# Kernel tuning notes

Hardware: AMD Instinct MI355X
Metric: run time of the kernel (lower is better)

Reference implementation:

```python
import jax, jax.numpy as jnp
import numpy as np

NEG = -1e9
TAU = 1.0
N_SAMPLES = 5
SWEEP = (0.1, 0.5, 5)


def layer_norm(x, g, b, eps=1e-5):
    m = x.mean(-1, keepdims=True)
    v = x.var(-1, keepdims=True)
    return (x - m) / jnp.sqrt(v + eps) * g + b


def entmax15(z):
    # exact 1.5-entmax along last axis (Peters & Martins 2019 sort-based algorithm)
    z = z / 2.0
    zs = jnp.sort(z, axis=-1)[..., ::-1]               # descending
    T = z.shape[-1]
    kk = jnp.arange(1, T + 1, dtype=z.dtype)
    mean = jnp.cumsum(zs, -1) / kk
    mean_sq = jnp.cumsum(zs * zs, -1) / kk
    ss = kk * (mean_sq - mean * mean)
    delta = jnp.clip((1.0 - ss) / kk, 0.0)
    tau = mean - jnp.sqrt(delta)
    support = jnp.sum((tau <= zs).astype(jnp.int32), -1, keepdims=True)  # k_star
    tau_star = jnp.take_along_axis(tau, support - 1, axis=-1)
    return jnp.square(jnp.clip(z - tau_star, 0.0))


def stochastic_topk(key, scores, attn, k, tau, n_samples):
    # vectorized over samples AND batch rows with per-row variable k:
    # threshold = k-th largest perturbed score per row (ties measure-zero w/ gumbel)
    u = jax.random.uniform(key, (n_samples,) + scores.shape)
    noise = -jnp.log(-jnp.log(u + 1e-6) + 1e-6)
    pert = jnp.where(attn[None] == 0, NEG, scores[None] + noise * tau)  # [S,B,T]
    srt = jnp.sort(pert, -1)[..., ::-1]
    idx = jnp.broadcast_to((k - 1)[None, :, None], pert.shape[:2] + (1,))
    thr = jnp.take_along_axis(srt, idx, axis=-1)       # [S,B,1]
    h = (pert >= thr).astype(scores.dtype)
    return h.mean(0)                                   # [B,T]


def pool(tok, attn):
    # masked mean pooling (stand-in for sent_encoder.pool)
    return (tok * attn[..., None]).sum(1) / jnp.clip(attn.sum(1, keepdims=True), 1e-6)


def _forward(ids, embeddings, attn, ln_g, ln_b, W1, b1, W2, b2, emb_table):
    emb = embeddings * attn[..., None]
    h = jax.nn.gelu(layer_norm(emb, ln_g, ln_b) @ W1 + b1, approximate=False)
    scores = (h @ W2 + b2)[..., 0]                     # [B,T]
    scores = jnp.where(attn == 0, NEG, scores)

    tok = emb_table[ids]                               # stand-in token embeddings
    full_rep = jax.lax.stop_gradient(pool(tok, attn))  # torch.no_grad path

    T_eff = attn.sum(1)                                # [B]
    # g_soft is identical across the rho sweep in the original; hoisted here
    g_soft = entmax15(scores / TAU) * attn
    g_soft = g_soft / jnp.clip(g_soft.sum(1, keepdims=True), 1e-6)

    key = jax.random.key(42)
    rhos = np.linspace(*SWEEP)
    g_sweep, loss_sweep, rho_eff_sweep = [], [], []
    recon_sum = jnp.zeros((), embeddings.dtype)
    g = None
    for j, rho in enumerate(rhos):
        k = jnp.maximum((float(rho) * T_eff).astype(jnp.int32), 1)
        g_hard = stochastic_topk(jax.random.fold_in(key, j), scores, attn, k, TAU, N_SAMPLES)
        # straight-through: hard forward, soft (entmax) backward
        g = jax.lax.stop_gradient(g_hard) - jax.lax.stop_gradient(g_soft) + g_soft
        rho_eff_sweep.append(g.sum(1) / T_eff)
        eff_attn = attn * g
        pred_rep = pool(tok, eff_attn)
        l_r = jnp.mean(jnp.square(pred_rep - full_rep))  # recon_loss = MSE stand-in
        recon_sum = recon_sum + l_r
        g_sweep.append(g)
        loss_sweep.append(l_r)
    recon_avg = recon_sum / len(rhos)
    return g, jnp.stack(g_sweep), recon_avg, jnp.stack(loss_sweep), jnp.stack(rho_eff_sweep)


def setup_inputs() -> dict:
    key = jax.random.key(0)
    B, T, D, H, V = 8, 2048, 1024, 1365, 32000
    ks = jax.random.split(key, 8)
    return {
        "ids": jax.random.randint(ks[0], (B, T), 0, V),
        "embeddings": jax.random.normal(ks[1], (B, T, D), jnp.float32),
        "attn": jnp.ones((B, T), jnp.float32),
        "ln_g": jnp.ones((D,), jnp.float32),
        "ln_b": jnp.zeros((D,), jnp.float32),
        "W1": jax.random.normal(ks[2], (D, H), jnp.float32) * 0.02,
        "b1": jnp.zeros((H,), jnp.float32),
        "W2": jax.random.normal(ks[3], (H, 1), jnp.float32) * 0.02,
        "b2": jnp.zeros((1,), jnp.float32),
        "emb_table": jax.random.normal(ks[4], (V, D), jnp.float32) * 0.02,
    }


def reference(ids, embeddings, attn, ln_g, ln_b, W1, b1, W2, b2, emb_table):
    return _forward(ids, embeddings, attn, ln_g, ln_b, W1, b1, W2, b2, emb_table)
```

## Files before the change

kernel.cpp:

```cpp
#include <hip/hip_runtime.h>
#include <math.h>
#include <stdint.h>

#define B_ 8
#define T_ 2048
#define D_ 1024
#define H_ 1365
#define HPAD 1536
#define NTOK (B_*T_)
#define NSAMP 5
#define NRHO 5

typedef float  f32x4  __attribute__((ext_vector_type(4)));
typedef __bf16 bf16x8 __attribute__((ext_vector_type(8)));

#define WS_SCORES 0
#define WS_CNT    (WS_SCORES + NTOK*8)
#define WS_PREDW  (WS_CNT + NRHO*B_*T_*4)
#define WS_FULLW  (WS_PREDW + NRHO*B_*D_*8)
#define WS_SUMEFF (WS_FULLW + B_*D_*8)
#define WS_SUMATT (WS_SUMEFF + NRHO*B_*8)
#define WS_SUMG   (WS_SUMATT + B_*8)
#define WS_ZERO_BYTES (WS_SUMG + NRHO*B_*8)
#define WS_STATS  (WS_SUMG + NRHO*B_*8)
#define WS_W1THI  (WS_STATS + NTOK*8)
#define WS_W1TLO  (WS_W1THI + (size_t)HPAD*D_*2)
#define WS_AHI    (WS_W1TLO + (size_t)HPAD*D_*2)
#define WS_ALO    (WS_AHI + (size_t)NTOK*D_*2)
#define WS_FULL_END (WS_ALO + (size_t)NTOK*D_*2)

#define OUT_G      0
#define OUT_GSW    16384
#define OUT_RECON  98304
#define OUT_LOSS   98305
#define OUT_RHOEFF 98310

__device__ inline unsigned short f2bf(float x) {
    uint32_t u = __float_as_uint(x);
    return (unsigned short)((u + 0x7FFFu + ((u >> 16) & 1u)) >> 16);
}

__launch_bounds__(256)
__global__ void k_w1t(const float* __restrict__ W1, unsigned short* __restrict__ hi,
                      unsigned short* __restrict__ lo)
{
    __shared__ float tile[32][33];
    const int tid = threadIdx.x;
    const int bk = blockIdx.x & 31;
    const int bh = blockIdx.x >> 5;
    const int k0 = bk * 32, h0 = bh * 32;
    const int a = tid & 31, b = tid >> 5;
    #pragma unroll
    for (int i = 0; i < 4; ++i) {
        int k = k0 + b + i * 8;
        int h = h0 + a;
        tile[b + i*8][a] = (h < H_) ? W1[(size_t)k * H_ + h] : 0.0f;
    }
    __syncthreads();
    #pragma unroll
    for (int i = 0; i < 4; ++i) {
        int hrow = h0 + b + i * 8;
        int kcol = k0 + a;
        float v = tile[a][b + i*8];
        unsigned short hb = f2bf(v);
        float hf = __uint_as_float((uint32_t)hb << 16);
        unsigned short lb = f2bf(v - hf);
        size_t dst = (size_t)hrow * D_ + kcol;
        hi[dst] = hb; lo[dst] = lb;
    }
}

__launch_bounds__(256)
__global__ void k_asplit(const float* __restrict__ emb, const float* __restrict__ attn,
                         const float* __restrict__ ln_g, const float* __restrict__ ln_b,
                         unsigned short* __restrict__ ahi, unsigned short* __restrict__ alo)
{
    const int tid = threadIdx.x, l = tid & 63, w = tid >> 6;
    const int t0 = blockIdx.x * 64;
    for (int tk = w; tk < 64; tk += 4) {
        const int tg = t0 + tk;
        const float av = attn[tg];
        const float* row = emb + (size_t)tg * D_;
        float rv[16];
        double s1 = 0.0, s2 = 0.0;
        #pragma unroll
        for (int i = 0; i < 16; ++i) {
            rv[i] = row[i*64 + l];
            double x = (double)rv[i] * (double)av;
            s1 += x; s2 += x * x;
        }
        for (int m = 32; m; m >>= 1) { s1 += __shfl_xor(s1, m); s2 += __shfl_xor(s2, m); }
        double mean = s1 / (double)D_;
        double var  = s2 / (double)D_ - mean * mean;
        double inv  = 1.0 / sqrt(var + 1e-5);
        float sc  = (float)((double)av * inv);
        float nsh = -(float)(mean * inv);
        #pragma unroll
        for (int i = 0; i < 16; ++i) {
            int k = i * 64 + l;
            float t  = fmaf(rv[i], sc, nsh);
            float xn = fmaf(t, ln_g[k], ln_b[k]);
            unsigned short hb = f2bf(xn);
            float hf = __uint_as_float((uint32_t)hb << 16);
            size_t dst = (size_t)tg * D_ + k;
            ahi[dst] = hb;
            alo[dst] = f2bf(xn - hf);
        }
    }
}

__launch_bounds__(256)
__global__ void k_stats(const float* __restrict__ emb, const float* __restrict__ attn,
                        float2* __restrict__ stats)
{
    const int tid = threadIdx.x, l = tid & 63, w = tid >> 6;
    const int t0 = blockIdx.x * 64;
    for (int tk = w; tk < 64; tk += 4) {
        const int tg = t0 + tk;
        const float av = attn[tg];
        const float* row = emb + (size_t)tg * D_;
        double s1 = 0.0, s2 = 0.0;
        #pragma unroll
        for (int i = 0; i < D_/64; ++i) {
            double x = (double)row[i*64 + l] * (double)av;
            s1 += x; s2 += x * x;
        }
        for (int m = 32; m; m >>= 1) { s1 += __shfl_xor(s1, m); s2 += __shfl_xor(s2, m); }
        if (l == 0) {
            double mean = s1 / (double)D_;
            double var  = s2 / (double)D_ - mean * mean;
            double inv  = 1.0 / sqrt(var + 1e-5);
            stats[tg] = make_float2((float)((double)av * inv), (float)(mean * inv));
        }
    }
}

#define BUFU 24576
#define OFF_ALO 4096
#define OFF_BHI 8192
#define OFF_BLO 16384
#define KSTEPS 32

__device__ __forceinline__ void gll16(const unsigned short* g, unsigned short* l)
{
    __builtin_amdgcn_global_load_lds((const __attribute__((address_space(1))) void*)g,
                                     (__attribute__((address_space(3))) void*)l, 16, 0, 0);
}

__launch_bounds__(512, 2)
__global__ void k_scores8(const unsigned short* __restrict__ ahi,
                          const unsigned short* __restrict__ alo,
                          const unsigned short* __restrict__ w1thi,
                          const unsigned short* __restrict__ w1tlo,
                          const float* __restrict__ b1, const float* __restrict__ W2,
                          double* __restrict__ scores)
{
    __shared__ __align__(16) unsigned short smem[3*BUFU];

    const int tid = threadIdx.x;
    const int blk = blockIdx.x;
    const int lin = (blk & 7) * 96 + (blk >> 3);
    const int mm = lin / 6, hh = lin - mm * 6;
    const int t0 = mm * 128;
    const int h0 = hh * 256;

    const int l  = tid & 63, w = tid >> 6;
    const int wr = w >> 2, wcn = w & 3;
    const int lm = l & 15, lq = l >> 4;

    const int lrow  = l >> 2;
    const int lslot = (l & 3) ^ ((l >> 3) & 3);
    const unsigned short* sA_hi  = ahi   + (size_t)(t0 + w*16 + lrow) * D_ + lslot*8;
    const unsigned short* sA_lo  = alo   + (size_t)(t0 + w*16 + lrow) * D_ + lslot*8;
    const unsigned short* sB_hi0 = w1thi + (size_t)(h0 + w*32 + lrow) * D_ + lslot*8;
    const unsigned short* sB_hi1 = sB_hi0 + 16*D_;
    const unsigned short* sB_lo0 = w1tlo + (size_t)(h0 + w*32 + lrow) * D_ + lslot*8;
    const unsigned short* sB_lo1 = sB_lo0 + 16*D_;
    const int dAhi  = w*512,            dAlo  = OFF_ALO + w*512;
    const int dBhi0 = OFF_BHI + w*1024, dBhi1 = dBhi0 + 512;
    const int dBlo0 = OFF_BLO + w*1024, dBlo1 = dBlo0 + 512;

    const int sw8 = (lq ^ ((lm >> 1) & 3)) * 8;
    int offAh[4], offBh[4];
    #pragma unroll
    for (int r = 0; r < 4; ++r) offAh[r] = (wr*64 + r*16 + lm)*32 + sw8;
    #pragma unroll
    for (int c = 0; c < 4; ++c) offBh[c] = OFF_BHI + (wcn*64 + c*16 + lm)*32 + sw8;

    f32x4 acc[4][4];
    #pragma unroll
    for (int r = 0; r < 4; ++r)
        #pragma unroll
        for (int c = 0; c < 4; ++c) acc[r][c] = (f32x4){0.f, 0.f, 0.f, 0.f};

    gll16(sA_hi,       &smem[0*BUFU + dAhi]);
    gll16(sA_lo,       &smem[0*BUFU + dAlo]);
    gll16(sB_hi0,      &smem[0*BUFU + dBhi0]);
    gll16(sB_hi1,      &smem[0*BUFU + dBhi1]);
    gll16(sB_lo0,      &smem[0*BUFU + dBlo0]);
    gll16(sB_lo1,      &smem[0*BUFU + dBlo1]);
    gll16(sA_hi  + 32, &smem[1*BUFU + dAhi]);
    gll16(sA_lo  + 32, &smem[1*BUFU + dAlo]);
    gll16(sB_hi0 + 32, &smem[1*BUFU + dBhi0]);
    gll16(sB_hi1 + 32, &smem[1*BUFU + dBhi1]);
    gll16(sB_lo0 + 32, &smem[1*BUFU + dBlo0]);
    gll16(sB_lo1 + 32, &smem[1*BUFU + dBlo1]);
    asm volatile("s_waitcnt vmcnt(6)" ::: "memory");
    asm volatile("s_barrier" ::: "memory");

    #pragma unroll
    for (int t = 0; t < KSTEPS; ++t) {
        const int dbase = (t % 3) * BUFU;
        const int ebase = ((t + 2) % 3) * BUFU;
        const int stK   = (t + 2) * 32;
        if (t < KSTEPS - 2) {
            gll16(sA_hi  + stK, &smem[ebase + dAhi]);
            gll16(sA_lo  + stK, &smem[ebase + dAlo]);
            gll16(sB_hi0 + stK, &smem[ebase + dBhi0]);
            gll16(sB_hi1 + stK, &smem[ebase + dBhi1]);
            gll16(sB_lo0 + stK, &smem[ebase + dBlo0]);
            gll16(sB_lo1 + stK, &smem[ebase + dBlo1]);
        }
        bf16x8 ah[4], bh[4], bl[4], al[4];
        #pragma unroll
        for (int r = 0; r < 4; ++r) ah[r] = *(const bf16x8*)&smem[dbase + offAh[r]];
        #pragma unroll
        for (int c = 0; c < 4; ++c) bh[c] = *(const bf16x8*)&smem[dbase + offBh[c]];
        __builtin_amdgcn_s_setprio(1);
        #pragma unroll
        for (int r = 0; r < 4; ++r)
            #pragma unroll
            for (int c = 0; c < 4; ++c)
                acc[r][c] = __builtin_amdgcn_mfma_f32_16x16x32_bf16(ah[r], bh[c], acc[r][c], 0, 0, 0);
        #pragma unroll
        for (int c = 0; c < 4; ++c) bl[c] = *(const bf16x8*)&smem[dbase + offBh[c] + (OFF_BLO - OFF_BHI)];
        #pragma unroll
        for (int r = 0; r < 4; ++r)
            #pragma unroll
            for (int c = 0; c < 4; ++c)
                acc[r][c] = __builtin_amdgcn_mfma_f32_16x16x32_bf16(ah[r], bl[c], acc[r][c], 0, 0, 0);
        #pragma unroll
        for (int r = 0; r < 4; ++r) al[r] = *(const bf16x8*)&smem[dbase + offAh[r] + OFF_ALO];
        #pragma unroll
        for (int r = 0; r < 4; ++r)
            #pragma unroll
            for (int c = 0; c < 4; ++c)
                acc[r][c] = __builtin_amdgcn_mfma_f32_16x16x32_bf16(al[r], bh[c], acc[r][c], 0, 0, 0);
        __builtin_amdgcn_s_setprio(0);
        if (t < KSTEPS - 2)       asm volatile("s_waitcnt vmcnt(6)" ::: "memory");
        else if (t == KSTEPS - 2) asm volatile("s_waitcnt vmcnt(0)" ::: "memory");
        if (t < KSTEPS - 1)       asm volatile("s_barrier" ::: "memory");
    }

    float b1v[4], w2v[4];
    #pragma unroll
    for (int c = 0; c < 4; ++c) {
        int hg = h0 + wcn*64 + c*16 + lm;
        bool ok = (hg < H_);
        b1v[c] = ok ? b1[hg] : 0.0f;
        w2v[c] = ok ? W2[hg] : 0.0f;
    }
    const float is2 = 0.70710678118654752440f;
    #pragma unroll
    for (int r = 0; r < 4; ++r) {
        #pragma unroll
        for (int i = 0; i < 4; ++i) {
            float ps = 0.0f;
            #pragma unroll
            for (int c = 0; c < 4; ++c) {
                float z  = acc[r][c][i] + b1v[c];
                float gl = 0.5f * z * (1.0f + erff(z * is2));
                ps = fmaf(gl, w2v[c], ps);
            }
            double psd = (double)ps;
            psd += __shfl_xor(psd, 1);
            psd += __shfl_xor(psd, 2);
            psd += __shfl_xor(psd, 4);
            psd += __shfl_xor(psd, 8);
            if (lm == 0)
                atomicAdd(&scores[t0 + wr*64 + r*16 + lq*4 + i], psd);
        }
    }
}

__launch_bounds__(256)
__global__ void k_scores_fb(const float* __restrict__ emb, const float* __restrict__ ln_g,
                            const float* __restrict__ ln_b, const float2* __restrict__ stats,
                            const unsigned short* __restrict__ w1thi,
                            const unsigned short* __restrict__ w1tlo,
                            const float* __restrict__ b1, const float* __restrict__ W2,
                            double* __restrict__ scores)
{
    __shared__ __align__(16) unsigned short sAhi[128*40];
    __shared__ __align__(16) unsigned short sAlo[128*40];
    __shared__ __align__(16) unsigned short sBhi[128*40];
    __shared__ __align__(16) unsigned short sBlo[128*40];
    __shared__ float sS1[128], sS2[128];

    const int tid = threadIdx.x;
    const int blk = blockIdx.x;
    const int xcd = blk & 7, slot = blk >> 3;
    const int lin = xcd * 176 + slot;
    const int tt = lin / 11, hh = lin - tt * 11;
    const int t0 = tt * 128;
    const int h0 = hh * 128;

    if (tid < 128) {
        float2 st = stats[t0 + tid];
        sS1[tid] = st.x; sS2[tid] = st.y;
    }
    f32x4 acc[4][4];
    #pragma unroll
    for (int r = 0; r < 4; ++r)
        #pragma unroll
        for (int c = 0; c < 4; ++c) acc[r][c] = (f32x4){0.f, 0.f, 0.f, 0.f};
    const int l = tid & 63, w = tid >> 6;
    const int lm = l & 15, lq = l >> 4;
    const int wr = (w >> 1) * 64;
    const int wc = (w & 1) * 64;
    __syncthreads();

    for (int kc = 0; kc < D_; kc += 32) {
        #pragma unroll
        for (int r2 = 0; r2 < 2; ++r2) {
            int g = tid + r2 * 256;
            int row = g >> 2, oct = g & 3;
            size_t src = (size_t)(h0 + row) * D_ + kc + oct * 8;
            int dst = row * 40 + oct * 8;
            *(bf16x8*)&sBhi[dst] = *(const bf16x8*)&w1thi[src];
            *(bf16x8*)&sBlo[dst] = *(const bf16x8*)&w1tlo[src];
        }
        #pragma unroll
        for (int r2 = 0; r2 < 2; ++r2) {
            int g = tid + r2 * 256;
            int tk = g >> 2, oct = g & 3;
            int tg = t0 + tk, dg = kc + oct * 8;
            const float* ep = emb + (size_t)tg * D_ + dg;
            float s1 = sS1[tk], ns2 = -sS2[tk];
            union { unsigned short s[8]; bf16x8 v; } hi, lo;
            #pragma unroll
            for (int j = 0; j < 8; ++j) {
                float t  = fmaf(ep[j], s1, ns2);
                float xn = fmaf(t, ln_g[dg + j], ln_b[dg + j]);
                unsigned short hb = f2bf(xn);
                float hf = __uint_as_float((uint32_t)hb << 16);
                hi.s[j] = hb;
                lo.s[j] = f2bf(xn - hf);
            }
            int dst = tk * 40 + oct * 8;
            *(bf16x8*)&sAhi[dst] = hi.v;
            *(bf16x8*)&sAlo[dst] = lo.v;
        }
        __syncthreads();
        bf16x8 ah[4], al[4], bh[4], bl[4];
        #pragma unroll
        for (int r = 0; r < 4; ++r) {
            int off = (wr + r * 16 + lm) * 40 + lq * 8;
            ah[r] = *(const bf16x8*)&sAhi[off];
            al[r] = *(const bf16x8*)&sAlo[off];
        }
        #pragma unroll
        for (int c = 0; c < 4; ++c) {
            int off = (wc + c * 16 + lm) * 40 + lq * 8;
            bh[c] = *(const bf16x8*)&sBhi[off];
            bl[c] = *(const bf16x8*)&sBlo[off];
        }
        #pragma unroll
        for (int r = 0; r < 4; ++r)
            #pragma unroll
            for (int c = 0; c < 4; ++c) {
                acc[r][c] = __builtin_amdgcn_mfma_f32_16x16x32_bf16(ah[r], bh[c], acc[r][c], 0, 0, 0);
                acc[r][c] = __builtin_amdgcn_mfma_f32_16x16x32_bf16(ah[r], bl[c], acc[r][c], 0, 0, 0);
                acc[r][c] = __builtin_amdgcn_mfma_f32_16x16x32_bf16(al[r], bh[c], acc[r][c], 0, 0, 0);
            }
        __syncthreads();
    }
    float b1v[4], w2v[4];
    #pragma unroll
    for (int c = 0; c < 4; ++c) {
        int hg = h0 + wc + c * 16 + lm;
        bool ok = (hg < H_);
        b1v[c] = ok ? b1[hg] : 0.0f;
        w2v[c] = ok ? W2[hg] : 0.0f;
    }
    const float is2 = 0.70710678118654752440f;
    #pragma unroll
    for (int r = 0; r < 4; ++r) {
        #pragma unroll
        for (int i = 0; i < 4; ++i) {
            float ps = 0.0f;
            #pragma unroll
            for (int c = 0; c < 4; ++c) {
                float z  = acc[r][c][i] + b1v[c];
                float gl = 0.5f * z * (1.0f + erff(z * is2));
                ps = fmaf(gl, w2v[c], ps);
            }
            double psd = (double)ps;
            psd += __shfl_xor(psd, 1);
            psd += __shfl_xor(psd, 2);
            psd += __shfl_xor(psd, 4);
            psd += __shfl_xor(psd, 8);
            if (lm == 0)
                atomicAdd(&scores[t0 + wr + r * 16 + lq * 4 + i], psd);
        }
    }
}

__device__ inline void tf2x32(uint32_t k0, uint32_t k1, uint32_t x0, uint32_t x1,
                              uint32_t& o0, uint32_t& o1)
{
    const uint32_t ks2 = k0 ^ k1 ^ 0x1BD11BDAu;
    x0 += k0; x1 += k1;
#define ROT_(v,d) (((v) << (d)) | ((v) >> (32 - (d))))
#define RND_(R) { x0 += x1; x1 = ROT_(x1, R); x1 ^= x0; }
    RND_(13) RND_(15) RND_(26) RND_(6)
    x0 += k1;  x1 += ks2 + 1u;
    RND_(17) RND_(29) RND_(16) RND_(24)
    x0 += ks2; x1 += k0 + 2u;
    RND_(13) RND_(15) RND_(26) RND_(6)
    x0 += k0;  x1 += k1 + 3u;
    RND_(17) RND_(29) RND_(16) RND_(24)
    x0 += k1;  x1 += ks2 + 4u;
    RND_(13) RND_(15) RND_(26) RND_(6)
    x0 += ks2; x1 += k0 + 5u;
    o0 = x0; o1 = x1;
#undef RND_
#undef ROT_
}

__launch_bounds__(256)
__global__ void k_topk(const double* __restrict__ scores, const float* __restrict__ attn,
                       const float* __restrict__ b2, int* __restrict__ cnt)
{
    __shared__ unsigned long long keys[2048];
    __shared__ unsigned int hist[256];
    __shared__ unsigned int wsum[4];
    __shared__ unsigned int selDigit, selBase;
    __shared__ double red[4];

    const int tid = threadIdx.x;
    const int blk = blockIdx.x;
    const int j = blk / 40;
    const int s = (blk % 40) >> 3;
    const int b = blk & 7;

    uint32_t kk0, kk1;
    tf2x32(0u, 42u, 0u, (uint32_t)j, kk0, kk1);

    double tsum = 0.0;
    for (int t = tid; t < T_; t += 256) tsum += (double)attn[b * T_ + t];
    for (int m = 32; m; m >>= 1) tsum += __shfl_xor(tsum, m);
    if ((tid & 63) == 0) red[tid >> 6] = tsum;
    __syncthreads();
    const double Teff = red[0] + red[1] + red[2] + red[3];
    const float rhos[5] = {0.1f, 0.2f, 0.3f, 0.4f, 0.5f};
    int kst = (int)(rhos[j] * (float)Teff);
    if (kst < 1) kst = 1;

    const double bb2 = (double)b2[0];
    #pragma unroll
    for (int r = 0; r < 8; ++r) {
        int t = tid + r * 256;
        int f = (s * 8 + b) * T_ + t;
        uint32_t o0, o1;
        tf2x32(kk0, kk1, 0u, (uint32_t)f, o0, o1);
        uint32_t bits = o0 ^ o1;
        float u = __uint_as_float((bits >> 9) | 0x3f800000u) - 1.0f;
        float a1 = (float)((double)u + (double)1e-6f);
        float la = (float)log((double)a1);
        float m1 = (float)((double)1e-6f - (double)la);
        float lb = (float)log((double)m1);
        float noise = -lb;
        float av = attn[b * T_ + t];
        double pv = (av == 0.0f) ? -1e9 : (scores[b * T_ + t] + bb2 + (double)noise);
        unsigned long long uu = (unsigned long long)__double_as_longlong(pv);
        keys[t] = (uu >> 63) ? ~uu : (uu | 0x8000000000000000ull);
    }
    __syncthreads();

    unsigned long long pfx = 0;
    unsigned int plo = (unsigned int)(2048 - kst);
    const int lane = tid & 63, wv = tid >> 6;
    for (int pass = 0; pass < 8; ++pass) {
        const int shift = 56 - 8 * pass;
        const unsigned long long maskhi = (pass == 0) ? 0ull : (~0ull << (64 - 8 * pass));
        hist[tid] = 0;
        __syncthreads();
        #pragma unroll
        for (int r = 0; r < 8; ++r) {
            unsigned long long kk = keys[tid + r * 256];
            if ((kk & maskhi) == pfx)
                atomicAdd(&hist[(unsigned int)((kk >> shift) & 255ull)], 1u);
        }
        __syncthreads();
        unsigned int own = hist[tid];
        int val = (int)own;
        #pragma unroll
        for (int off = 1; off < 64; off <<= 1) {
            int n = __shfl_up(val, off);
            if (lane >= off) val += n;
        }
        if (lane == 63) wsum[wv] = (unsigned int)val;
        __syncthreads();
        unsigned int woff = 0;
        for (int q = 0; q < wv; ++q) woff += wsum[q];
        unsigned int incl = (unsigned int)val + woff;
        unsigned int excl = incl - own;
        if (own > 0 && plo >= excl && plo < incl) { selDigit = (unsigned int)tid; selBase = excl; }
        __syncthreads();
        pfx |= ((unsigned long long)selDigit << shift);
        plo -= selBase;
        __syncthreads();
    }

    #pragma unroll
    for (int r = 0; r < 8; ++r) {
        int t = tid + r * 256;
        if (keys[t] >= pfx) atomicAdd(&cnt[(j * 8 + b) * T_ + t], 1);
    }
}

__launch_bounds__(256)
__global__ void k_gfin(const int* __restrict__ cnt, const float* __restrict__ attn,
                       float* __restrict__ out, double* __restrict__ sumeff,
                       double* __restrict__ sumatt, double* __restrict__ sumg)
{
    __shared__ double redA[4], redB[4], redC[4];
    const int j = blockIdx.x >> 3, b = blockIdx.x & 7;
    const int tid = threadIdx.x;
    double sg = 0.0, se = 0.0, sa = 0.0;
    for (int t = tid; t < T_; t += 256) {
        int c = cnt[(j * 8 + b) * T_ + t];
        float g  = (float)c / 5.0f;
        float av = attn[b * T_ + t];
        out[OUT_GSW + (j * 8 + b) * T_ + t] = g;
        if (j == 4) out[OUT_G + b * T_ + t] = g;
        sg += (double)g;
        se += (double)(av * g);
        sa += (double)av;
    }
    for (int m = 32; m; m >>= 1) { sg += __shfl_xor(sg, m); se += __shfl_xor(se, m); sa += __shfl_xor(sa, m); }
    if ((tid & 63) == 0) { redA[tid>>6] = sg; redB[tid>>6] = se; redC[tid>>6] = sa; }
    __syncthreads();
    if (tid == 0) {
        sg = redA[0]+redA[1]+redA[2]+redA[3];
        se = redB[0]+redB[1]+redB[2]+redB[3];
        sa = redC[0]+redC[1]+redC[2]+redC[3];
        sumg[j*8+b] = sg; sumeff[j*8+b] = se;
        if (j == 0) sumatt[b] = sa;
        out[OUT_RHOEFF + j*8 + b] = (float)sg / (float)sa;
    }
}

__launch_bounds__(256)
__global__ void k_pool(const int* __restrict__ ids, const float* __restrict__ attn,
                       const float* __restrict__ out, const float* __restrict__ emb_table,
                       double* __restrict__ predw, double* __restrict__ fullw)
{
    __shared__ int   sid[128];
    __shared__ float sw[6][128];
    const int blk = blockIdx.x;
    const int b  = blk >> 6;
    const int dc = (blk >> 4) & 3;
    const int tc = blk & 15;
    const int tid = threadIdx.x;
    const int d = dc * 256 + tid;
    if (tid < 128) {
        int t = tc * 128 + tid;
        sid[tid] = ids[b * T_ + t];
        float av = attn[b * T_ + t];
        sw[0][tid] = av;
        #pragma unroll
        for (int j = 0; j < 5; ++j) {
            float g = out[OUT_GSW + (j * 8 + b) * T_ + t];
            sw[1 + j][tid] = av * g;
        }
    }
    __syncthreads();
    double acc[6] = {0,0,0,0,0,0};
    for (int i = 0; i < 128; ++i) {
        float val = emb_table[(size_t)sid[i] * D_ + d];
        #pragma unroll
        for (int c = 0; c < 6; ++c) acc[c] += (double)(val * sw[c][i]);
    }
    atomicAdd(&fullw[b * D_ + d], acc[0]);
    #pragma unroll
    for (int j = 0; j < 5; ++j)
        atomicAdd(&predw[(j * 8 + b) * D_ + d], acc[1 + j]);
}

__launch_bounds__(256)
__global__ void k_loss(const double* __restrict__ predw, const double* __restrict__ fullw,
                       const double* __restrict__ sumeff, const double* __restrict__ sumatt,
                       float* __restrict__ out)
{
    __shared__ double red[4];
    __shared__ float lr[5];
    const int tid = threadIdx.x;
    for (int j = 0; j < 5; ++j) {
        double p = 0.0;
        for (int i = tid; i < B_ * D_; i += 256) {
            int b = i >> 10;
            double dF = sumatt[b];        if (dF < 1e-6) dF = 1e-6;
            double dE = sumeff[j*8 + b];  if (dE < 1e-6) dE = 1e-6;
            double diff = predw[j * B_ * D_ + i] / dE - fullw[i] / dF;
            p += diff * diff;
        }
        for (int m = 32; m; m >>= 1) p += __shfl_xor(p, m);
        if ((tid & 63) == 0) red[tid >> 6] = p;
        __syncthreads();
        if (tid == 0) {
            double t = red[0] + red[1] + red[2] + red[3];
            lr[j] = (float)(t / (double)(B_ * D_));
            out[OUT_LOSS + j] = lr[j];
        }
        __syncthreads();
    }
    if (tid == 0) {
        float srec = 0.0f;
        for (int j = 0; j < 5; ++j) srec += lr[j];
        out[OUT_RECON] = srec / 5.0f;
    }
}

extern "C" void kernel_launch(void* const* d_in, const int* in_sizes, int n_in,
                              void* d_out, int out_size, void* d_ws, size_t ws_size,
                              hipStream_t stream)
{
    const int*   ids  = (const int*)  d_in[0];
    const float* emb  = (const float*)d_in[1];
    const float* attn = (const float*)d_in[2];
    const float* ln_g = (const float*)d_in[3];
    const float* ln_b = (const float*)d_in[4];
    const float* W1   = (const float*)d_in[5];
    const float* b1   = (const float*)d_in[6];
    const float* W2   = (const float*)d_in[7];
    const float* b2   = (const float*)d_in[8];
    const float* et   = (const float*)d_in[9];
    float* out = (float*)d_out;
    char*  ws  = (char*)d_ws;

    double* scores = (double*)(ws + WS_SCORES);
    int*    cnt    = (int*)   (ws + WS_CNT);
    double* predw  = (double*)(ws + WS_PREDW);
    double* fullw  = (double*)(ws + WS_FULLW);
    double* sumeff = (double*)(ws + WS_SUMEFF);
    double* sumatt = (double*)(ws + WS_SUMATT);
    double* sumg   = (double*)(ws + WS_SUMG);
    float2* stats  = (float2*)(ws + WS_STATS);
    unsigned short* w1thi = (unsigned short*)(ws + WS_W1THI);
    unsigned short* w1tlo = (unsigned short*)(ws + WS_W1TLO);
    unsigned short* ahi   = (unsigned short*)(ws + WS_AHI);
    unsigned short* alo   = (unsigned short*)(ws + WS_ALO);

    hipMemsetAsync(d_ws, 0, WS_ZERO_BYTES, stream);

    k_w1t<<<48*32, 256, 0, stream>>>(W1, w1thi, w1tlo);
    if (ws_size >= WS_FULL_END) {
        k_asplit<<<NTOK/64, 256, 0, stream>>>(emb, attn, ln_g, ln_b, ahi, alo);
        k_scores8<<<768, 512, 0, stream>>>(ahi, alo, w1thi, w1tlo, b1, W2, scores);
    } else {
        k_stats<<<NTOK/64, 256, 0, stream>>>(emb, attn, stats);
        k_scores_fb<<<1408, 256, 0, stream>>>(emb, ln_g, ln_b, stats, w1thi, w1tlo,
                                              b1, W2, scores);
    }
    k_topk<<<NRHO * NSAMP * B_, 256, 0, stream>>>(scores, attn, b2, cnt);
    k_gfin<<<NRHO * B_, 256, 0, stream>>>(cnt, attn, out, sumeff, sumatt, sumg);
    k_pool<<<512, 256, 0, stream>>>(ids, attn, out, et, predw, fullw);
    k_loss<<<1, 256, 0, stream>>>(predw, fullw, sumeff, sumatt, out);
}
```

Baseline: 495.9 us.

## Split hi/lo LDS rings and prefetch next hi fragments into registers

Splits the shared-memory staging into a 4-deep ring for the hi-precision A/B tiles and a 2-deep ring for the lo tiles, so hi data is fetched three steps ahead. The hi fragments for the next k-step are loaded into double-buffered registers during the current step, which moves LDS read latency off the MFMA critical path. The lo tiles get only one step of global-load lead, which may expose memory latency. The larger register footprint may also pressure occupancy under the 512x2 launch bounds.

```diff
diff --git a/kernel.cpp b/kernel.cpp
--- a/kernel.cpp
+++ b/kernel.cpp
@@ -135,10 +135,9 @@
     }
 }
 
-#define BUFU 24576
-#define OFF_ALO 4096
-#define OFF_BHI 8192
-#define OFF_BLO 16384
+#define HIBUF_U 12288
+#define LOBUF_U 12288
+#define LORING0 49152
 #define KSTEPS 32
 
 __device__ __forceinline__ void gll16(const unsigned short* g, unsigned short* l)
@@ -155,7 +154,7 @@
                           const float* __restrict__ b1, const float* __restrict__ W2,
                           double* __restrict__ scores)
 {
-    __shared__ __align__(16) unsigned short smem[3*BUFU];
+    __shared__ __align__(16) unsigned short smem[LORING0 + 2*LOBUF_U];
 
     const int tid = threadIdx.x;
     const int blk = blockIdx.x;
@@ -176,16 +175,15 @@
     const unsigned short* sB_hi1 = sB_hi0 + 16*D_;
     const unsigned short* sB_lo0 = w1tlo + (size_t)(h0 + w*32 + lrow) * D_ + lslot*8;
     const unsigned short* sB_lo1 = sB_lo0 + 16*D_;
-    const int dAhi  = w*512,            dAlo  = OFF_ALO + w*512;
-    const int dBhi0 = OFF_BHI + w*1024, dBhi1 = dBhi0 + 512;
-    const int dBlo0 = OFF_BLO + w*1024, dBlo1 = dBlo0 + 512;
+    const int dA  = w*512;
+    const int dB0 = 4096 + w*1024, dB1 = dB0 + 512;
 
     const int sw8 = (lq ^ ((lm >> 1) & 3)) * 8;
-    int offAh[4], offBh[4];
-    #pragma unroll
-    for (int r = 0; r < 4; ++r) offAh[r] = (wr*64 + r*16 + lm)*32 + sw8;
-    #pragma unroll
-    for (int c = 0; c < 4; ++c) offBh[c] = OFF_BHI + (wcn*64 + c*16 + lm)*32 + sw8;
+    int offA[4], offB[4];
+    #pragma unroll
+    for (int r = 0; r < 4; ++r) offA[r] = (wr*64 + r*16 + lm)*32 + sw8;
+    #pragma unroll
+    for (int c = 0; c < 4; ++c) offB[c] = 4096 + (wcn*64 + c*16 + lm)*32 + sw8;
 
     f32x4 acc[4][4];
     #pragma unroll
@@ -193,63 +191,77 @@
         #pragma unroll
         for (int c = 0; c < 4; ++c) acc[r][c] = (f32x4){0.f, 0.f, 0.f, 0.f};
 
-    gll16(sA_hi,       &smem[0*BUFU + dAhi]);
-    gll16(sA_lo,       &smem[0*BUFU + dAlo]);
-    gll16(sB_hi0,      &smem[0*BUFU + dBhi0]);
-    gll16(sB_hi1,      &smem[0*BUFU + dBhi1]);
-    gll16(sB_lo0,      &smem[0*BUFU + dBlo0]);
-    gll16(sB_lo1,      &smem[0*BUFU + dBlo1]);
-    gll16(sA_hi  + 32, &smem[1*BUFU + dAhi]);
-    gll16(sA_lo  + 32, &smem[1*BUFU + dAlo]);
-    gll16(sB_hi0 + 32, &smem[1*BUFU + dBhi0]);
-    gll16(sB_hi1 + 32, &smem[1*BUFU + dBhi1]);
-    gll16(sB_lo0 + 32, &smem[1*BUFU + dBlo0]);
-    gll16(sB_lo1 + 32, &smem[1*BUFU + dBlo1]);
-    asm volatile("s_waitcnt vmcnt(6)" ::: "memory");
+    gll16(sA_hi,       &smem[0*HIBUF_U + dA]);
+    gll16(sB_hi0,      &smem[0*HIBUF_U + dB0]);
+    gll16(sB_hi1,      &smem[0*HIBUF_U + dB1]);
+    gll16(sA_lo,       &smem[LORING0 + dA]);
+    gll16(sB_lo0,      &smem[LORING0 + dB0]);
+    gll16(sB_lo1,      &smem[LORING0 + dB1]);
+    gll16(sA_hi  + 32, &smem[1*HIBUF_U + dA]);
+    gll16(sB_hi0 + 32, &smem[1*HIBUF_U + dB0]);
+    gll16(sB_hi1 + 32, &smem[1*HIBUF_U + dB1]);
+    gll16(sA_hi  + 64, &smem[2*HIBUF_U + dA]);
+    gll16(sB_hi0 + 64, &smem[2*HIBUF_U + dB0]);
+    gll16(sB_hi1 + 64, &smem[2*HIBUF_U + dB1]);
+    asm volatile("s_waitcnt vmcnt(3)" ::: "memory");
     asm volatile("s_barrier" ::: "memory");
 
+    bf16x8 ahp[2][4], bhp[2][4];
+    #pragma unroll
+    for (int r = 0; r < 4; ++r) ahp[0][r] = *(const bf16x8*)&smem[offA[r]];
+    #pragma unroll
+    for (int c = 0; c < 4; ++c) bhp[0][c] = *(const bf16x8*)&smem[offB[c]];
+
     #pragma unroll
     for (int t = 0; t < KSTEPS; ++t) {
-        const int dbase = (t % 3) * BUFU;
-        const int ebase = ((t + 2) % 3) * BUFU;
-        const int stK   = (t + 2) * 32;
-        if (t < KSTEPS - 2) {
-            gll16(sA_hi  + stK, &smem[ebase + dAhi]);
-            gll16(sA_lo  + stK, &smem[ebase + dAlo]);
-            gll16(sB_hi0 + stK, &smem[ebase + dBhi0]);
-            gll16(sB_hi1 + stK, &smem[ebase + dBhi1]);
-            gll16(sB_lo0 + stK, &smem[ebase + dBlo0]);
-            gll16(sB_lo1 + stK, &smem[ebase + dBlo1]);
-        }
-        bf16x8 ah[4], bh[4], bl[4], al[4];
-        #pragma unroll
-        for (int r = 0; r < 4; ++r) ah[r] = *(const bf16x8*)&smem[dbase + offAh[r]];
-        #pragma unroll
-        for (int c = 0; c < 4; ++c) bh[c] = *(const bf16x8*)&smem[dbase + offBh[c]];
+        const int cur = t & 1, nxt = (t + 1) & 1;
+        const int lobase = LORING0 + (t & 1) * LOBUF_U;
+        if (t + 1 < KSTEPS) {
+            const int lb = LORING0 + ((t + 1) & 1) * LOBUF_U;
+            const int ko = (t + 1) * 32;
+            gll16(sA_lo  + ko, &smem[lb + dA]);
+            gll16(sB_lo0 + ko, &smem[lb + dB0]);
+            gll16(sB_lo1 + ko, &smem[lb + dB1]);
+        }
+        if (t + 3 < KSTEPS) {
+            const int hb = ((t + 3) & 3) * HIBUF_U;
+            const int ko = (t + 3) * 32;
+            gll16(sA_hi  + ko, &smem[hb + dA]);
+            gll16(sB_hi0 + ko, &smem[hb + dB0]);
+            gll16(sB_hi1 + ko, &smem[hb + dB1]);
+        }
+        bf16x8 bl[4], al[4];
+        #pragma unroll
+        for (int c = 0; c < 4; ++c) bl[c] = *(const bf16x8*)&smem[lobase + offB[c]];
+        #pragma unroll
+        for (int r = 0; r < 4; ++r) al[r] = *(const bf16x8*)&smem[lobase + offA[r]];
+        if (t + 1 < KSTEPS) {
+            const int hb = ((t + 1) & 3) * HIBUF_U;
+            #pragma unroll
+            for (int r = 0; r < 4; ++r) ahp[nxt][r] = *(const bf16x8*)&smem[hb + offA[r]];
+            #pragma unroll
+            for (int c = 0; c < 4; ++c) bhp[nxt][c] = *(const bf16x8*)&smem[hb + offB[c]];
+        }
         __builtin_amdgcn_s_setprio(1);
         #pragma unroll
         for (int r = 0; r < 4; ++r)
             #pragma unroll
             for (int c = 0; c < 4; ++c)
-                acc[r][c] = __builtin_amdgcn_mfma_f32_16x16x32_bf16(ah[r], bh[c], acc[r][c], 0, 0, 0);
-        #pragma unroll
-        for (int c = 0; c < 4; ++c) bl[c] = *(const bf16x8*)&smem[dbase + offBh[c] + (OFF_BLO - OFF_BHI)];
+                acc[r][c] = __builtin_amdgcn_mfma_f32_16x16x32_bf16(ahp[cur][r], bhp[cur][c], acc[r][c], 0, 0, 0);
         #pragma unroll
         for (int r = 0; r < 4; ++r)
             #pragma unroll
             for (int c = 0; c < 4; ++c)
-                acc[r][c] = __builtin_amdgcn_mfma_f32_16x16x32_bf16(ah[r], bl[c], acc[r][c], 0, 0, 0);
-        #pragma unroll
-        for (int r = 0; r < 4; ++r) al[r] = *(const bf16x8*)&smem[dbase + offAh[r] + OFF_ALO];
+                acc[r][c] = __builtin_amdgcn_mfma_f32_16x16x32_bf16(ahp[cur][r], bl[c], acc[r][c], 0, 0, 0);
         #pragma unroll
         for (int r = 0; r < 4; ++r)
             #pragma unroll
             for (int c = 0; c < 4; ++c)
-                acc[r][c] = __builtin_amdgcn_mfma_f32_16x16x32_bf16(al[r], bh[c], acc[r][c], 0, 0, 0);
+                acc[r][c] = __builtin_amdgcn_mfma_f32_16x16x32_bf16(al[r], bhp[cur][c], acc[r][c], 0, 0, 0);
         __builtin_amdgcn_s_setprio(0);
-        if (t < KSTEPS - 2)       asm volatile("s_waitcnt vmcnt(6)" ::: "memory");
-        else if (t == KSTEPS - 2) asm volatile("s_waitcnt vmcnt(0)" ::: "memory");
-        if (t < KSTEPS - 1)       asm volatile("s_barrier" ::: "memory");
+        if (t < KSTEPS - 3)      asm volatile("s_waitcnt vmcnt(3)" ::: "memory");
+        else if (t < KSTEPS - 1) asm volatile("s_waitcnt vmcnt(0)" ::: "memory");
+        if (t < KSTEPS - 1)      asm volatile("s_barrier" ::: "memory");
     }
 
     float b1v[4], w2v[4];
```

Measured after the change: 489.5 us. About the same (-1.3%).
